# Performance work log

Measured on AMD Instinct MI355X. Metric: run time of the kernel, lower is better.

Reference implementation:

```python
import jax, jax.numpy as jnp
import numpy as np

EPS = 1e-5

def _conv1x1(x, w, b):
    # x: [B,C,H,W], w: [O,C], b: [O]  (1x1 conv == channel matmul)
    return jnp.einsum('bchw,oc->bohw', x, w) + b[None, :, None, None]

def _bn_relu(y, gamma, beta, mean, var):
    inv = gamma / jnp.sqrt(var + EPS)
    return jax.nn.relu(y * inv[None, :, None, None] + (beta - mean * inv)[None, :, None, None])

def setup_inputs() -> dict:
    key = jax.random.key(0)
    ks = jax.random.split(key, 8)
    B, C, H, W = 8, 2048, 48, 48
    mid = C // 4  # k = 4 -> mid_ch = 512
    s_in = (2.0 / C) ** 0.5   # kaiming-like scale for 1x1 convs from C channels
    s_mid = (2.0 / mid) ** 0.5
    return {
        'x': jax.random.normal(ks[0], (B, C, H, W), jnp.float32),
        'f_w': jax.random.normal(ks[1], (mid, C), jnp.float32) * s_in,
        'f_b': jnp.zeros((mid,), jnp.float32),
        'f_gamma': jnp.ones((mid,), jnp.float32),
        'f_beta': jnp.zeros((mid,), jnp.float32),
        'f_mean': jnp.zeros((mid,), jnp.float32),
        'f_var': jnp.ones((mid,), jnp.float32),
        'g_w': jax.random.normal(ks[2], (mid, C), jnp.float32) * s_in,
        'g_b': jnp.zeros((mid,), jnp.float32),
        'g_gamma': jnp.ones((mid,), jnp.float32),
        'g_beta': jnp.zeros((mid,), jnp.float32),
        'g_mean': jnp.zeros((mid,), jnp.float32),
        'g_var': jnp.ones((mid,), jnp.float32),
        'h_w': jax.random.normal(ks[3], (mid, C), jnp.float32) * s_in,
        'h_b': jnp.zeros((mid,), jnp.float32),
        'v_w': jax.random.normal(ks[4], (C, mid), jnp.float32) * s_mid,
        'v_b': jnp.zeros((C,), jnp.float32),
    }

def reference(x, f_w, f_b, f_gamma, f_beta, f_mean, f_var,
              g_w, g_b, g_gamma, g_beta, g_mean, g_var,
              h_w, h_b, v_w, v_b):
    B, C, H, W = x.shape
    mid = f_w.shape[0]
    N = H * W
    f_x = _bn_relu(_conv1x1(x, f_w, f_b), f_gamma, f_beta, f_mean, f_var).reshape(B, mid, N)
    g_x = _bn_relu(_conv1x1(x, g_w, g_b), g_gamma, g_beta, g_mean, g_var).reshape(B, mid, N)
    h_x = _conv1x1(x, h_w, h_b).reshape(B, mid, N)
    # z = f_x^T @ g_x : [B, N, N]
    scores = jnp.einsum('bcn,bcm->bnm', f_x, g_x) * (mid ** -0.5)
    attn = jax.nn.softmax(scores, axis=-1)
    # z = attn @ h_x^T : [B, N, mid] -> [B, mid, H, W]
    z = jnp.einsum('bnm,bcm->bcn', attn, h_x).reshape(B, mid, H, W)
    z = jnp.einsum('bchw,oc->bohw', z, v_w) + v_b[None, :, None, None]
    return (z + x, attn)
```

## Files before the change

kernel.cpp:

```cpp
#include <hip/hip_runtime.h>
#include <math.h>

typedef unsigned short u16;
typedef unsigned short u16x8 __attribute__((ext_vector_type(8)));
typedef __bf16 bf16x8 __attribute__((ext_vector_type(8)));
typedef float f32x4 __attribute__((ext_vector_type(4)));

typedef __attribute__((address_space(1))) const unsigned int gu32;
typedef __attribute__((address_space(3))) unsigned int su32;

#define B_ 8
#define C_ 2048
#define MID_ 512
#define N_ 2304

#define BAR() do { asm volatile("" ::: "memory"); __builtin_amdgcn_s_barrier(); asm volatile("" ::: "memory"); } while (0)

#define QMFMA(AV, BV, MO, NO)                                                             \
  { _Pragma("unroll") for (int mfi = 0; mfi < 4; ++mfi) {                                 \
      _Pragma("unroll") for (int nfi = 0; nfi < 2; ++nfi) {                               \
        acc[MO + mfi][NO + nfi] = __builtin_amdgcn_mfma_f32_16x16x32_bf16(                \
            AV[0][mfi], BV[0][nfi], acc[MO + mfi][NO + nfi], 0, 0, 0);                    \
        acc[MO + mfi][NO + nfi] = __builtin_amdgcn_mfma_f32_16x16x32_bf16(                \
            AV[1][mfi], BV[1][nfi], acc[MO + mfi][NO + nfi], 0, 0, 0); } } }

static __device__ __forceinline__ u16 f2bf(float f) {
  union { float f; unsigned u; } c; c.f = f;
  unsigned u = c.u;
  u += 0x7fffu + ((u >> 16) & 1u);
  return (u16)(u >> 16);
}
static __device__ __forceinline__ float bf2f(u16 x) {
  union { unsigned u; float f; } c; c.u = ((unsigned)x) << 16; return c.f;
}

__global__ __launch_bounds__(256) void prep_wall_k(
    const float* __restrict__ fw, const float* __restrict__ gw,
    const float* __restrict__ hw, u16* __restrict__ wall) {
  int idx = blockIdx.x * 256 + threadIdx.x;
  if (idx >= 1536 * 2048) return;
  int r = idx >> 11;
  float v = (r < 512) ? fw[idx] : (r < 1024) ? gw[idx - (512 << 11)] : hw[idx - (1024 << 11)];
  wall[idx] = f2bf(v);
}

__global__ __launch_bounds__(256) void prep_vw_k(const float* __restrict__ vw, u16* __restrict__ o) {
  int idx = blockIdx.x * 256 + threadIdx.x;
  if (idx < 2048 * 512) o[idx] = f2bf(vw[idx]);
}

__global__ __launch_bounds__(256) void prep_sb_k(
    const float* fb, const float* fg, const float* fbe, const float* fm, const float* fv,
    const float* gb, const float* gg, const float* gbe, const float* gm, const float* gv,
    const float* hb, float* __restrict__ scale, float* __restrict__ bias) {
  int i = blockIdx.x * 256 + threadIdx.x;
  if (i >= 1536) return;
  const float FS = 0.044194173824159216f;
  if (i < 512) {
    float inv = fg[i] / sqrtf(fv[i] + 1e-5f);
    scale[i] = inv * FS; bias[i] = (fb[i] * inv + fbe[i] - fm[i] * inv) * FS;
  } else if (i < 1024) {
    int j = i - 512;
    float inv = gg[j] / sqrtf(gv[j] + 1e-5f);
    scale[i] = inv; bias[i] = gb[j] * inv + gbe[j] - gm[j] * inv;
  } else {
    scale[i] = 1.0f; bias[i] = hb[i - 1024];
  }
}

__global__ __launch_bounds__(256) void transpose_x_k(const float* __restrict__ x, u16* __restrict__ xT) {
  __shared__ float tile[64][68];
  const int b = blockIdx.z;
  const int n0 = blockIdx.x * 64, c0 = blockIdx.y * 64;
  const float* xb = x + (size_t)b * C_ * N_;
  u16* xTb = xT + (size_t)b * N_ * C_;
  const int r = threadIdx.x >> 2, q = threadIdx.x & 3;
  #pragma unroll
  for (int j = 0; j < 4; ++j) {
    float4 v = *(const float4*)&xb[(size_t)(c0 + r) * N_ + n0 + (q + 4 * j) * 4];
    *(float4*)&tile[r][(q + 4 * j) * 4] = v;
  }
  __syncthreads();
  #pragma unroll
  for (int g = 0; g < 2; ++g) {
    const int cl = (q * 2 + g) * 8;
    u16x8 w;
    #pragma unroll
    for (int e = 0; e < 8; ++e) w[e] = f2bf(tile[cl + e][r]);
    *(u16x8*)&xTb[(size_t)(n0 + r) * C_ + c0 + cl] = w;
  }
}

__global__ __launch_bounds__(256) void transpose_h_k(const u16* __restrict__ fghT, u16* __restrict__ hx) {
  __shared__ u16 tile[32][33];
  const int b = blockIdx.z;
  const int n0 = blockIdx.x * 32, c0 = blockIdx.y * 32;
  const u16* src = fghT + (size_t)b * N_ * 1536;
  u16* dst = hx + (size_t)b * MID_ * N_;
  const int tx = threadIdx.x & 31, ty = threadIdx.x >> 5;
  #pragma unroll
  for (int i = 0; i < 4; ++i)
    tile[ty + i * 8][tx] = src[(size_t)(n0 + ty + i * 8) * 1536 + 1024 + c0 + tx];
  __syncthreads();
  #pragma unroll
  for (int i = 0; i < 4; ++i)
    dst[(size_t)(c0 + ty + i * 8) * N_ + n0 + tx] = tile[tx][ty + i * 8];
}

#define EP_FG 0
#define EP_SCALE16 1
#define EP_FINAL 2

template<int EPI, int SWZ, int GX, int GY>
__global__ __launch_bounds__(512, 2) void gemm5_kernel(
    const u16* __restrict__ Ag, int lda, long long sA,
    const u16* __restrict__ Bg, int ldb, long long sB,
    void* __restrict__ Cg, int ldc, long long sC, int K,
    const float* __restrict__ ep_scale, const float* __restrict__ ep_bias,
    const float* __restrict__ ep_x, long long sX)
{
  extern __shared__ __align__(16) u16 smem[];
  u16* As = smem;
  u16* Bs = smem + 2 * 256 * 64;

  int tx, ty, tz;
  {
    const int L = blockIdx.x;
    const int xcd = L & 7, r = L >> 3;
    if constexpr (SWZ == 0) {
      const int i = r % GX, j = (r / GX) * 8 + xcd;
      tx = i; ty = j % GY; tz = j / GY;
    } else if constexpr (SWZ == 1) {
      const int i = r % GY, j = (r / GY) * 8 + xcd;
      ty = i; tx = j % GX; tz = j / GX;
    } else {
      const int i = r % 9, jg = (r / 9) * 8 + xcd;
      const int bx = jg % (GX / 3), rem = jg / (GX / 3);
      const int by = rem % (GY / 3); tz = rem / (GY / 3);
      tx = bx * 3 + i % 3; ty = by * 3 + i / 3;
    }
  }

  const int tid = threadIdx.x;
  const int lane = tid & 63;
  const int wv = tid >> 6;
  const int b = tz;
  const int m0 = ty * 256;
  const int n0 = tx * 256;
  const int wm = (wv >> 2) * 128;
  const int wn = (wv & 3) * 64;
  const int lr = lane & 15, lg = lane >> 4;

  const u16* Ab = Ag + (size_t)b * sA;
  const u16* Bb = Bg + (size_t)b * sB;
  const int nk = K >> 6;

  const int srow = lane >> 3;
  const int sksw = ((lane & 7) ^ srow) * 8;

  const int rdsw0 = ((0 + lg) ^ (lr & 7)) * 8;
  const int rdsw1 = ((4 + lg) ^ (lr & 7)) * 8;

  f32x4 acc[8][4];
  #pragma unroll
  for (int i = 0; i < 8; ++i)
    #pragma unroll
    for (int j = 0; j < 4; ++j)
      acc[i][j] = f32x4{0.f, 0.f, 0.f, 0.f};

  auto STAGE_A = [&](int p2, int t) {
    #pragma unroll
    for (int j = 0; j < 4; ++j) {
      const int rb = j * 64 + wv * 8;
      const u16* g = Ab + (size_t)(m0 + rb + srow) * lda + t * 64 + sksw;
      __builtin_amdgcn_global_load_lds((gu32*)g, (su32*)(As + p2 * 16384 + rb * 64), 16, 0, 0);
    }
  };
  auto STAGE_B = [&](int p2, int t) {
    #pragma unroll
    for (int j = 0; j < 4; ++j) {
      const int rb = j * 64 + wv * 8;
      const u16* g = Bb + (size_t)(n0 + rb + srow) * ldb + t * 64 + sksw;
      __builtin_amdgcn_global_load_lds((gu32*)g, (su32*)(Bs + p2 * 16384 + rb * 64), 16, 0, 0);
    }
  };

  STAGE_A(0, 0); STAGE_B(0, 0);
  if (nk > 1) { STAGE_A(1, 1); STAGE_B(1, 1); }

  for (int kt = 0; kt < nk; ++kt) {
    const int p = kt & 1;
    if (kt + 1 < nk) asm volatile("s_waitcnt vmcnt(8)" ::: "memory");
    else             asm volatile("s_waitcnt vmcnt(0)" ::: "memory");
    BAR();

    const u16* Asl = As + p * 16384;
    const u16* Bsl = Bs + p * 16384;
    const bool st = (kt + 2) < nk;
    const int ps = (kt + 2) & 1;

    bf16x8 aV[2][4], bLo[2][2], bHi[2][2];

    #pragma unroll
    for (int ks = 0; ks < 2; ++ks) {
      const int ro = ks ? rdsw1 : rdsw0;
      #pragma unroll
      for (int i = 0; i < 4; ++i)
        aV[ks][i] = *(const bf16x8*)(Asl + (wm + i * 16 + lr) * 64 + ro);
      #pragma unroll
      for (int i = 0; i < 2; ++i)
        bLo[ks][i] = *(const bf16x8*)(Bsl + (wn + i * 16 + lr) * 64 + ro);
    }
    BAR();
    __builtin_amdgcn_s_setprio(1);
    QMFMA(aV, bLo, 0, 0);
    __builtin_amdgcn_s_setprio(0);
    BAR();

    #pragma unroll
    for (int ks = 0; ks < 2; ++ks) {
      const int ro = ks ? rdsw1 : rdsw0;
      #pragma unroll
      for (int i = 0; i < 2; ++i)
        bHi[ks][i] = *(const bf16x8*)(Bsl + (wn + 32 + i * 16 + lr) * 64 + ro);
    }
    BAR();
    __builtin_amdgcn_s_setprio(1);
    QMFMA(aV, bHi, 0, 2);
    __builtin_amdgcn_s_setprio(0);
    BAR();

    #pragma unroll
    for (int ks = 0; ks < 2; ++ks) {
      const int ro = ks ? rdsw1 : rdsw0;
      #pragma unroll
      for (int i = 0; i < 4; ++i)
        aV[ks][i] = *(const bf16x8*)(Asl + (wm + 64 + i * 16 + lr) * 64 + ro);
    }
    if (st) STAGE_B(ps, kt + 2);
    BAR();
    __builtin_amdgcn_s_setprio(1);
    QMFMA(aV, bLo, 4, 0);
    __builtin_amdgcn_s_setprio(0);
    BAR();

    if (st) STAGE_A(ps, kt + 2);
    BAR();
    __builtin_amdgcn_s_setprio(1);
    QMFMA(aV, bHi, 4, 2);
    __builtin_amdgcn_s_setprio(0);
    BAR();
  }

  u16*   C16 = (u16*)Cg + (size_t)b * sC;
  float* C32 = (float*)Cg + (size_t)b * sC;
  const float* xb = (EPI == EP_FINAL) ? (ep_x + (size_t)b * sX) : nullptr;
  #pragma unroll
  for (int mf = 0; mf < 8; ++mf) {
    #pragma unroll
    for (int nf = 0; nf < 4; ++nf) {
      #pragma unroll
      for (int r = 0; r < 4; ++r) {
        int row = m0 + wm + mf * 16 + lg * 4 + r;
        int col = n0 + wn + nf * 16 + lr;
        float v = acc[mf][nf][r];
        if constexpr (EPI == EP_FG) {
          v = v * ep_scale[col] + ep_bias[col];
          if (col < 1024) v = fmaxf(v, 0.f);
          C16[(size_t)row * ldc + col] = f2bf(v);
        } else if constexpr (EPI == EP_SCALE16) {
          C16[(size_t)row * ldc + col] = f2bf(v);
        } else {
          v += ep_bias[row] + xb[(size_t)row * ldc + col];
          C32[(size_t)row * ldc + col] = v;
        }
      }
    }
  }
}

__global__ __launch_bounds__(256) void softmax_k(u16* __restrict__ SP, float* __restrict__ attn) {
  u16* sp = SP + (size_t)blockIdx.x * N_;
  float* ar = attn + (size_t)blockIdx.x * N_;
  const int tid = threadIdx.x;
  u16x8 s8 = *(const u16x8*)&sp[tid * 8];
  u16 st = sp[2048 + tid];
  float w[8], wt = bf2f(st);
  #pragma unroll
  for (int j = 0; j < 8; ++j) w[j] = bf2f(s8[j]);
  float mx = wt;
  #pragma unroll
  for (int j = 0; j < 8; ++j) mx = fmaxf(mx, w[j]);
  #pragma unroll
  for (int o = 32; o; o >>= 1) mx = fmaxf(mx, __shfl_xor(mx, o));
  __shared__ float red[4], red2[4];
  if ((tid & 63) == 0) red[tid >> 6] = mx;
  __syncthreads();
  mx = fmaxf(fmaxf(red[0], red[1]), fmaxf(red[2], red[3]));
  float s = 0.f;
  #pragma unroll
  for (int j = 0; j < 8; ++j) { w[j] = __expf(w[j] - mx); s += w[j]; }
  wt = __expf(wt - mx); s += wt;
  #pragma unroll
  for (int o = 32; o; o >>= 1) s += __shfl_xor(s, o);
  if ((tid & 63) == 0) red2[tid >> 6] = s;
  __syncthreads();
  s = red2[0] + red2[1] + red2[2] + red2[3];
  float inv = 1.0f / s;
  #pragma unroll
  for (int j = 0; j < 8; ++j) w[j] *= inv;
  wt *= inv;
  float4 o0 = {w[0], w[1], w[2], w[3]}, o1 = {w[4], w[5], w[6], w[7]};
  *(float4*)&ar[tid * 8] = o0;
  *(float4*)&ar[tid * 8 + 4] = o1;
  ar[2048 + tid] = wt;
  u16x8 p8;
  #pragma unroll
  for (int j = 0; j < 8; ++j) p8[j] = f2bf(w[j]);
  *(u16x8*)&sp[tid * 8] = p8;
  sp[2048 + tid] = f2bf(wt);
}

extern "C" void kernel_launch(void* const* d_in, const int* in_sizes, int n_in,
                              void* d_out, int out_size, void* d_ws, size_t ws_size,
                              hipStream_t stream) {
  const float* x    = (const float*)d_in[0];
  const float* f_w  = (const float*)d_in[1];
  const float* f_b  = (const float*)d_in[2];
  const float* f_ga = (const float*)d_in[3];
  const float* f_be = (const float*)d_in[4];
  const float* f_me = (const float*)d_in[5];
  const float* f_va = (const float*)d_in[6];
  const float* g_w  = (const float*)d_in[7];
  const float* g_b  = (const float*)d_in[8];
  const float* g_ga = (const float*)d_in[9];
  const float* g_be = (const float*)d_in[10];
  const float* g_me = (const float*)d_in[11];
  const float* g_va = (const float*)d_in[12];
  const float* h_w  = (const float*)d_in[13];
  const float* h_b  = (const float*)d_in[14];
  const float* v_w  = (const float*)d_in[15];
  const float* v_b  = (const float*)d_in[16];

  float* out0 = (float*)d_out;
  float* attn = out0 + (size_t)B_ * C_ * N_;

  char* p = (char*)d_ws;
  u16* xT   = (u16*)p; p += (size_t)B_ * N_ * C_ * 2;
  u16* fghT = (u16*)p; p += (size_t)B_ * N_ * 1536 * 2;
  u16* hx   = (u16*)p; p += (size_t)B_ * MID_ * N_ * 2;
  u16* ZT   = (u16*)p; p += (size_t)B_ * N_ * MID_ * 2;
  u16* Wall = (u16*)p; p += (size_t)1536 * C_ * 2;
  u16* vwb  = (u16*)p; p += (size_t)C_ * MID_ * 2;
  float* sc = (float*)p; p += 1536 * 4;
  float* bi = (float*)p; p += 1536 * 4;
  u16* SP   = (u16*)p; p += (size_t)B_ * N_ * N_ * 2;

  hipFuncSetAttribute((const void*)gemm5_kernel<EP_FG, 0, 6, 9>,      hipFuncAttributeMaxDynamicSharedMemorySize, 131072);
  hipFuncSetAttribute((const void*)gemm5_kernel<EP_SCALE16, 2, 9, 9>, hipFuncAttributeMaxDynamicSharedMemorySize, 131072);
  hipFuncSetAttribute((const void*)gemm5_kernel<EP_SCALE16, 0, 2, 9>, hipFuncAttributeMaxDynamicSharedMemorySize, 131072);
  hipFuncSetAttribute((const void*)gemm5_kernel<EP_FINAL, 1, 9, 8>,   hipFuncAttributeMaxDynamicSharedMemorySize, 131072);

  prep_wall_k<<<(1536 * 2048 + 255) / 256, 256, 0, stream>>>(f_w, g_w, h_w, Wall);
  prep_vw_k<<<(2048 * 512 + 255) / 256, 256, 0, stream>>>(v_w, vwb);
  prep_sb_k<<<6, 256, 0, stream>>>(f_b, f_ga, f_be, f_me, f_va,
                                   g_b, g_ga, g_be, g_me, g_va, h_b, sc, bi);
  transpose_x_k<<<dim3(N_ / 64, C_ / 64, B_), 256, 0, stream>>>(x, xT);

  gemm5_kernel<EP_FG, 0, 6, 9><<<dim3(6 * 9 * 8), 512, 131072, stream>>>(
      xT, C_, (long long)N_ * C_, Wall, C_, 0,
      fghT, 1536, (long long)N_ * 1536, C_, sc, bi, nullptr, 0);

  transpose_h_k<<<dim3(N_ / 32, MID_ / 32, B_), 256, 0, stream>>>(fghT, hx);

  gemm5_kernel<EP_SCALE16, 2, 9, 9><<<dim3(9 * 9 * 8), 512, 131072, stream>>>(
      fghT, 1536, (long long)N_ * 1536, fghT + 512, 1536, (long long)N_ * 1536,
      SP, N_, (long long)N_ * N_, MID_, nullptr, nullptr, nullptr, 0);

  softmax_k<<<B_ * N_, 256, 0, stream>>>(SP, attn);

  gemm5_kernel<EP_SCALE16, 0, 2, 9><<<dim3(2 * 9 * 8), 512, 131072, stream>>>(
      SP, N_, (long long)N_ * N_, hx, N_, (long long)MID_ * N_,
      ZT, MID_, (long long)N_ * MID_, N_, nullptr, nullptr, nullptr, 0);

  gemm5_kernel<EP_FINAL, 1, 9, 8><<<dim3(9 * 8 * 8), 512, 131072, stream>>>(
      vwb, MID_, 0, ZT, MID_, (long long)N_ * MID_,
      out0, N_, (long long)C_ * N_, MID_, nullptr, v_b, x, (long long)C_ * N_);
}
```

Before: 505.2 us.

## Merge prep kernels, vectorize h transpose, and use wave-per-row softmax

Merges the three weight and scale prep kernels into one launch that converts eight elements per thread with float4 loads and 16-byte stores. The h-transpose moves to 64x64 tiles with 16-byte loads and stores. Softmax now gives each 64-lane wave one row, removing the shared-memory reductions and block barriers. The SP buffer is aligned to 256 bytes so the wider vector accesses stay aligned. The aim is fewer launches and fewer, wider memory transactions in the small memory-bound kernels; the GEMMs, which dominate the runtime, are untouched.

```diff
diff --git a/kernel.cpp b/kernel.cpp
--- a/kernel.cpp
+++ b/kernel.cpp
@@ -2,6 +2,7 @@
 #include <math.h>
 
 typedef unsigned short u16;
+typedef unsigned short u16x4 __attribute__((ext_vector_type(4)));
 typedef unsigned short u16x8 __attribute__((ext_vector_type(8)));
 typedef __bf16 bf16x8 __attribute__((ext_vector_type(8)));
 typedef float f32x4 __attribute__((ext_vector_type(4)));
@@ -34,37 +35,44 @@
   union { unsigned u; float f; } c; c.u = ((unsigned)x) << 16; return c.f;
 }
 
-__global__ __launch_bounds__(256) void prep_wall_k(
+__global__ __launch_bounds__(256) void prep_all_k(
     const float* __restrict__ fw, const float* __restrict__ gw,
-    const float* __restrict__ hw, u16* __restrict__ wall) {
-  int idx = blockIdx.x * 256 + threadIdx.x;
-  if (idx >= 1536 * 2048) return;
-  int r = idx >> 11;
-  float v = (r < 512) ? fw[idx] : (r < 1024) ? gw[idx - (512 << 11)] : hw[idx - (1024 << 11)];
-  wall[idx] = f2bf(v);
-}
-
-__global__ __launch_bounds__(256) void prep_vw_k(const float* __restrict__ vw, u16* __restrict__ o) {
-  int idx = blockIdx.x * 256 + threadIdx.x;
-  if (idx < 2048 * 512) o[idx] = f2bf(vw[idx]);
-}
-
-__global__ __launch_bounds__(256) void prep_sb_k(
+    const float* __restrict__ hw, const float* __restrict__ vw,
     const float* fb, const float* fg, const float* fbe, const float* fm, const float* fv,
     const float* gb, const float* gg, const float* gbe, const float* gm, const float* gv,
-    const float* hb, float* __restrict__ scale, float* __restrict__ bias) {
-  int i = blockIdx.x * 256 + threadIdx.x;
-  if (i >= 1536) return;
-  const float FS = 0.044194173824159216f;
-  if (i < 512) {
-    float inv = fg[i] / sqrtf(fv[i] + 1e-5f);
-    scale[i] = inv * FS; bias[i] = (fb[i] * inv + fbe[i] - fm[i] * inv) * FS;
-  } else if (i < 1024) {
-    int j = i - 512;
-    float inv = gg[j] / sqrtf(gv[j] + 1e-5f);
-    scale[i] = inv; bias[i] = gb[j] * inv + gbe[j] - gm[j] * inv;
-  } else {
-    scale[i] = 1.0f; bias[i] = hb[i - 1024];
+    const float* hb,
+    u16* __restrict__ wall, u16* __restrict__ vwb,
+    float* __restrict__ scale, float* __restrict__ bias) {
+  const int gid = blockIdx.x * 256 + threadIdx.x;
+  if (gid < 393216) {
+    int e = gid * 8; int r = e >> 11;
+    const float* s = (r < 512) ? (fw + e) : (r < 1024) ? (gw + e - (512 << 11)) : (hw + e - (1024 << 11));
+    float4 v0 = *(const float4*)s, v1 = *(const float4*)(s + 4);
+    u16x8 w;
+    w[0]=f2bf(v0.x); w[1]=f2bf(v0.y); w[2]=f2bf(v0.z); w[3]=f2bf(v0.w);
+    w[4]=f2bf(v1.x); w[5]=f2bf(v1.y); w[6]=f2bf(v1.z); w[7]=f2bf(v1.w);
+    *(u16x8*)&wall[e] = w;
+  } else if (gid < 524288) {
+    int e = (gid - 393216) * 8;
+    float4 v0 = *(const float4*)(vw + e), v1 = *(const float4*)(vw + e + 4);
+    u16x8 w;
+    w[0]=f2bf(v0.x); w[1]=f2bf(v0.y); w[2]=f2bf(v0.z); w[3]=f2bf(v0.w);
+    w[4]=f2bf(v1.x); w[5]=f2bf(v1.y); w[6]=f2bf(v1.z); w[7]=f2bf(v1.w);
+    *(u16x8*)&vwb[e] = w;
+  }
+  if (gid < 1536) {
+    const float FS = 0.044194173824159216f;
+    int i = gid;
+    if (i < 512) {
+      float inv = fg[i] / sqrtf(fv[i] + 1e-5f);
+      scale[i] = inv * FS; bias[i] = (fb[i] * inv + fbe[i] - fm[i] * inv) * FS;
+    } else if (i < 1024) {
+      int j = i - 512;
+      float inv = gg[j] / sqrtf(gv[j] + 1e-5f);
+      scale[i] = inv; bias[i] = gb[j] * inv + gbe[j] - gm[j] * inv;
+    } else {
+      scale[i] = 1.0f; bias[i] = hb[i - 1024];
+    }
   }
 }
 
@@ -92,19 +100,26 @@
 }
 
 __global__ __launch_bounds__(256) void transpose_h_k(const u16* __restrict__ fghT, u16* __restrict__ hx) {
-  __shared__ u16 tile[32][33];
+  __shared__ u16 tile[64][72];
   const int b = blockIdx.z;
-  const int n0 = blockIdx.x * 32, c0 = blockIdx.y * 32;
+  const int n0 = blockIdx.x * 64, c0 = blockIdx.y * 64;
   const u16* src = fghT + (size_t)b * N_ * 1536;
   u16* dst = hx + (size_t)b * MID_ * N_;
-  const int tx = threadIdx.x & 31, ty = threadIdx.x >> 5;
-  #pragma unroll
-  for (int i = 0; i < 4; ++i)
-    tile[ty + i * 8][tx] = src[(size_t)(n0 + ty + i * 8) * 1536 + 1024 + c0 + tx];
+  const int r = threadIdx.x >> 2, q = threadIdx.x & 3;
+  #pragma unroll
+  for (int g = 0; g < 2; ++g) {
+    const int cl = q * 16 + g * 8;
+    *(u16x8*)&tile[r][cl] = *(const u16x8*)&src[(size_t)(n0 + r) * 1536 + 1024 + c0 + cl];
+  }
   __syncthreads();
   #pragma unroll
-  for (int i = 0; i < 4; ++i)
-    dst[(size_t)(c0 + ty + i * 8) * N_ + n0 + tx] = tile[tx][ty + i * 8];
+  for (int g = 0; g < 2; ++g) {
+    const int cl = q * 16 + g * 8;
+    u16x8 w;
+    #pragma unroll
+    for (int e = 0; e < 8; ++e) w[e] = tile[cl + e][r];
+    *(u16x8*)&dst[(size_t)(c0 + r) * N_ + n0 + cl] = w;
+  }
 }
 
 #define EP_FG 0
@@ -157,7 +172,6 @@
 
   const int srow = lane >> 3;
   const int sksw = ((lane & 7) ^ srow) * 8;
-
   const int rdsw0 = ((0 + lg) ^ (lr & 7)) * 8;
   const int rdsw1 = ((4 + lg) ^ (lr & 7)) * 8;
 
@@ -280,45 +294,53 @@
 }
 
 __global__ __launch_bounds__(256) void softmax_k(u16* __restrict__ SP, float* __restrict__ attn) {
-  u16* sp = SP + (size_t)blockIdx.x * N_;
-  float* ar = attn + (size_t)blockIdx.x * N_;
-  const int tid = threadIdx.x;
-  u16x8 s8 = *(const u16x8*)&sp[tid * 8];
-  u16 st = sp[2048 + tid];
-  float w[8], wt = bf2f(st);
-  #pragma unroll
-  for (int j = 0; j < 8; ++j) w[j] = bf2f(s8[j]);
-  float mx = wt;
-  #pragma unroll
-  for (int j = 0; j < 8; ++j) mx = fmaxf(mx, w[j]);
+  const int l = threadIdx.x & 63;
+  const size_t row = (size_t)blockIdx.x * 4 + (threadIdx.x >> 6);
+  u16* sp = SP + row * N_;
+  float* ar = attn + row * N_;
+
+  u16x8 s[4];
+  #pragma unroll
+  for (int j = 0; j < 4; ++j) s[j] = *(const u16x8*)&sp[j * 512 + l * 8];
+  u16x4 st4 = *(const u16x4*)&sp[2048 + l * 4];
+
+  float v[4][8], t[4];
+  float mx = -3.0e38f;
+  #pragma unroll
+  for (int j = 0; j < 4; ++j)
+    #pragma unroll
+    for (int e = 0; e < 8; ++e) { v[j][e] = bf2f(s[j][e]); mx = fmaxf(mx, v[j][e]); }
+  #pragma unroll
+  for (int e = 0; e < 4; ++e) { t[e] = bf2f(st4[e]); mx = fmaxf(mx, t[e]); }
   #pragma unroll
   for (int o = 32; o; o >>= 1) mx = fmaxf(mx, __shfl_xor(mx, o));
-  __shared__ float red[4], red2[4];
-  if ((tid & 63) == 0) red[tid >> 6] = mx;
-  __syncthreads();
-  mx = fmaxf(fmaxf(red[0], red[1]), fmaxf(red[2], red[3]));
-  float s = 0.f;
-  #pragma unroll
-  for (int j = 0; j < 8; ++j) { w[j] = __expf(w[j] - mx); s += w[j]; }
-  wt = __expf(wt - mx); s += wt;
-  #pragma unroll
-  for (int o = 32; o; o >>= 1) s += __shfl_xor(s, o);
-  if ((tid & 63) == 0) red2[tid >> 6] = s;
-  __syncthreads();
-  s = red2[0] + red2[1] + red2[2] + red2[3];
-  float inv = 1.0f / s;
-  #pragma unroll
-  for (int j = 0; j < 8; ++j) w[j] *= inv;
-  wt *= inv;
-  float4 o0 = {w[0], w[1], w[2], w[3]}, o1 = {w[4], w[5], w[6], w[7]};
-  *(float4*)&ar[tid * 8] = o0;
-  *(float4*)&ar[tid * 8 + 4] = o1;
-  ar[2048 + tid] = wt;
-  u16x8 p8;
-  #pragma unroll
-  for (int j = 0; j < 8; ++j) p8[j] = f2bf(w[j]);
-  *(u16x8*)&sp[tid * 8] = p8;
-  sp[2048 + tid] = f2bf(wt);
+
+  float sum = 0.f;
+  #pragma unroll
+  for (int j = 0; j < 4; ++j)
+    #pragma unroll
+    for (int e = 0; e < 8; ++e) { v[j][e] = __expf(v[j][e] - mx); sum += v[j][e]; }
+  #pragma unroll
+  for (int e = 0; e < 4; ++e) { t[e] = __expf(t[e] - mx); sum += t[e]; }
+  #pragma unroll
+  for (int o = 32; o; o >>= 1) sum += __shfl_xor(sum, o);
+  const float inv = 1.0f / sum;
+
+  #pragma unroll
+  for (int j = 0; j < 4; ++j) {
+    float4 lo = {v[j][0] * inv, v[j][1] * inv, v[j][2] * inv, v[j][3] * inv};
+    float4 hi = {v[j][4] * inv, v[j][5] * inv, v[j][6] * inv, v[j][7] * inv};
+    *(float4*)&ar[j * 512 + l * 8] = lo;
+    *(float4*)&ar[j * 512 + l * 8 + 4] = hi;
+    u16x8 p8;
+    p8[0]=f2bf(lo.x); p8[1]=f2bf(lo.y); p8[2]=f2bf(lo.z); p8[3]=f2bf(lo.w);
+    p8[4]=f2bf(hi.x); p8[5]=f2bf(hi.y); p8[6]=f2bf(hi.z); p8[7]=f2bf(hi.w);
+    *(u16x8*)&sp[j * 512 + l * 8] = p8;
+  }
+  float4 tl = {t[0] * inv, t[1] * inv, t[2] * inv, t[3] * inv};
+  *(float4*)&ar[2048 + l * 4] = tl;
+  u16x4 p4; p4[0]=f2bf(tl.x); p4[1]=f2bf(tl.y); p4[2]=f2bf(tl.z); p4[3]=f2bf(tl.w);
+  *(u16x4*)&sp[2048 + l * 4] = p4;
 }
 
 extern "C" void kernel_launch(void* const* d_in, const int* in_sizes, int n_in,
@@ -354,6 +376,7 @@
   u16* vwb  = (u16*)p; p += (size_t)C_ * MID_ * 2;
   float* sc = (float*)p; p += 1536 * 4;
   float* bi = (float*)p; p += 1536 * 4;
+  p = (char*)(((size_t)p + 255) & ~(size_t)255);
   u16* SP   = (u16*)p; p += (size_t)B_ * N_ * N_ * 2;
 
   hipFuncSetAttribute((const void*)gemm5_kernel<EP_FG, 0, 6, 9>,      hipFuncAttributeMaxDynamicSharedMemorySize, 131072);
@@ -361,23 +384,23 @@
   hipFuncSetAttribute((const void*)gemm5_kernel<EP_SCALE16, 0, 2, 9>, hipFuncAttributeMaxDynamicSharedMemorySize, 131072);
   hipFuncSetAttribute((const void*)gemm5_kernel<EP_FINAL, 1, 9, 8>,   hipFuncAttributeMaxDynamicSharedMemorySize, 131072);
 
-  prep_wall_k<<<(1536 * 2048 + 255) / 256, 256, 0, stream>>>(f_w, g_w, h_w, Wall);
-  prep_vw_k<<<(2048 * 512 + 255) / 256, 256, 0, stream>>>(v_w, vwb);
-  prep_sb_k<<<6, 256, 0, stream>>>(f_b, f_ga, f_be, f_me, f_va,
-                                   g_b, g_ga, g_be, g_me, g_va, h_b, sc, bi);
+  prep_all_k<<<2048, 256, 0, stream>>>(f_w, g_w, h_w, v_w,
+                                       f_b, f_ga, f_be, f_me, f_va,
+                                       g_b, g_ga, g_be, g_me, g_va, h_b,
+                                       Wall, vwb, sc, bi);
   transpose_x_k<<<dim3(N_ / 64, C_ / 64, B_), 256, 0, stream>>>(x, xT);
 
   gemm5_kernel<EP_FG, 0, 6, 9><<<dim3(6 * 9 * 8), 512, 131072, stream>>>(
       xT, C_, (long long)N_ * C_, Wall, C_, 0,
       fghT, 1536, (long long)N_ * 1536, C_, sc, bi, nullptr, 0);
 
-  transpose_h_k<<<dim3(N_ / 32, MID_ / 32, B_), 256, 0, stream>>>(fghT, hx);
+  transpose_h_k<<<dim3(N_ / 64, MID_ / 64, B_), 256, 0, stream>>>(fghT, hx);
 
   gemm5_kernel<EP_SCALE16, 2, 9, 9><<<dim3(9 * 9 * 8), 512, 131072, stream>>>(
       fghT, 1536, (long long)N_ * 1536, fghT + 512, 1536, (long long)N_ * 1536,
       SP, N_, (long long)N_ * N_, MID_, nullptr, nullptr, nullptr, 0);
 
-  softmax_k<<<B_ * N_, 256, 0, stream>>>(SP, attn);
+  softmax_k<<<(B_ * N_) / 4, 256, 0, stream>>>(SP, attn);
 
   gemm5_kernel<EP_SCALE16, 0, 2, 9><<<dim3(2 * 9 * 8), 512, 131072, stream>>>(
       SP, N_, (long long)N_ * N_, hx, N_, (long long)MID_ * N_,
```

New measurement: 504.3 us. About the same (-0.2%).
